# Performance work log

Measured on AMD Instinct MI355X. Metric: run time of the kernel, lower is better.

Reference implementation:

```python
import jax, jax.numpy as jnp
import numpy as np

HIDDEN = 2048
NUM_INPUTS = 4
ACTIVE_IDX = 0
EPS = 1e-6


def rms_norm(x, scale, eps=EPS):
    # Gemma3n RMSNorm: compute in float32, scale by learned per-channel weight.
    x32 = x.astype(jnp.float32)
    inv = jax.lax.rsqrt(jnp.mean(x32 * x32, axis=-1, keepdims=True) + eps)
    return (x32 * inv * scale.astype(jnp.float32)).astype(x.dtype)


def compute_modalities(x, router_norm_scale, router_w):
    # router_norm -> * hidden_size**-1 -> Dense(N) -> tanh (in fp32)
    router_inputs = rms_norm(x, router_norm_scale) * (1.0 / HIDDEN)
    routed = jnp.einsum('bsh,hn->bsn', router_inputs, router_w)
    return jnp.tanh(routed.astype(jnp.float32)).astype(x.dtype)


def setup_inputs() -> dict:
    key = jax.random.key(0)
    k = jax.random.split(key, 7)
    N, B, S, H = NUM_INPUTS, 4, 2048, HIDDEN
    return {
        'hidden_states': jax.random.normal(k[0], (N, B, S, H), dtype=jnp.float32),
        'activated': jax.random.normal(k[1], (B, S, H), dtype=jnp.float32),
        'router_norm_scale': jnp.ones((H,), dtype=jnp.float32) + 0.02 * jax.random.normal(k[2], (H,), dtype=jnp.float32),
        'router_w': 0.02 * jax.random.normal(k[3], (H, N), dtype=jnp.float32),
        'pred_w': 0.02 * jax.random.normal(k[4], (N, N * N), dtype=jnp.float32),
        'corr_w': 0.02 * jax.random.normal(k[5], (N, N), dtype=jnp.float32),
        'correct_output_scale': jax.random.normal(k[6], (H,), dtype=jnp.float32),
    }


def reference(hidden_states, activated, router_norm_scale, router_w, pred_w, corr_w, correct_output_scale):
    N = NUM_INPUTS
    B, S, H = activated.shape

    # ---- predict ----
    mod_p = compute_modalities(hidden_states[ACTIVE_IDX], router_norm_scale, router_w)  # [B,S,N]
    raw = jnp.einsum('bsn,nk->bsk', mod_p, pred_w).reshape(B, S, N, N)  # [B,S,N,N]
    # keras: transpose(raw,(0,1,3,2)) then matmul(hs^(1,2,3,0), .) then transpose back
    # predictions[m,b,s,h] = sum_n hs[n,b,s,h] * raw[b,s,m,n]
    predictions = jnp.einsum('nbsh,bsmn->mbsh', hidden_states, raw) + hidden_states

    # ---- correct ----
    mod_c = compute_modalities(activated, router_norm_scale, router_w)  # [B,S,N]
    innovation = activated - predictions[ACTIVE_IDX]  # [B,S,H]
    coefs = jnp.einsum('bsn,nm->bsm', mod_c, corr_w) + 1.0  # [B,S,N]
    corrected = predictions + innovation[None] * jnp.transpose(coefs, (2, 0, 1))[..., None]

    # ---- scale_corrected_output ----
    return corrected * correct_output_scale
```

## Files before the change

### kernel.cpp

```cpp
#include <hip/hip_runtime.h>

#define HID 2048
#define NTHREADS 256

__global__ __launch_bounds__(NTHREADS) void altup_fused(
    const float* __restrict__ hs,
    const float* __restrict__ act,
    const float* __restrict__ rns,
    const float* __restrict__ rw,
    const float* __restrict__ pw,
    const float* __restrict__ cw,
    const float* __restrict__ cscale,
    float* __restrict__ out,
    int T)
{
    const int t   = blockIdx.x;
    const int tid = threadIdx.x;
    const int h0  = tid * 8;

    __shared__ float s_red[4][10];
    __shared__ float s_raw[16];
    __shared__ float s_coef[4];

    const size_t tok = (size_t)t * HID;
    const size_t strideN = (size_t)T * HID;

    float x0v[8], av[8], nsv[8], wl[32];
    *(float4*)(x0v + 0) = *(const float4*)(hs  + tok + h0 + 0);
    *(float4*)(x0v + 4) = *(const float4*)(hs  + tok + h0 + 4);
    *(float4*)(av  + 0) = *(const float4*)(act + tok + h0 + 0);
    *(float4*)(av  + 4) = *(const float4*)(act + tok + h0 + 4);
    *(float4*)(nsv + 0) = *(const float4*)(rns + h0 + 0);
    *(float4*)(nsv + 4) = *(const float4*)(rns + h0 + 4);
    #pragma unroll
    for (int q = 0; q < 8; ++q)
        *(float4*)(wl + q * 4) = *(const float4*)(rw + (size_t)h0 * 4 + q * 4);

    float r[10];
    #pragma unroll
    for (int k = 0; k < 10; ++k) r[k] = 0.f;
    #pragma unroll
    for (int j = 0; j < 8; ++j) {
        float x0 = x0v[j];
        float a  = av[j];
        float ns = nsv[j];
        r[0] += x0 * x0;
        r[1] += a * a;
        float xs = x0 * ns, as_ = a * ns;
        #pragma unroll
        for (int n = 0; n < 4; ++n) {
            float w = wl[j * 4 + n];
            r[2 + n] += xs  * w;
            r[6 + n] += as_ * w;
        }
    }

    #pragma unroll
    for (int off = 32; off > 0; off >>= 1) {
        #pragma unroll
        for (int k = 0; k < 10; ++k) r[k] += __shfl_down(r[k], off, 64);
    }
    const int wave = tid >> 6, lane = tid & 63;
    if (lane == 0) {
        #pragma unroll
        for (int k = 0; k < 10; ++k) s_red[wave][k] = r[k];
    }
    __syncthreads();

    if (tid == 0) {
        float acc[10];
        #pragma unroll
        for (int k = 0; k < 10; ++k)
            acc[k] = s_red[0][k] + s_red[1][k] + s_red[2][k] + s_red[3][k];
        const float invH = 1.0f / (float)HID;
        float inv_p = rsqrtf(acc[0] * invH + 1e-6f);
        float inv_c = rsqrtf(acc[1] * invH + 1e-6f);
        float mp[4], mc[4];
        #pragma unroll
        for (int n = 0; n < 4; ++n) {
            mp[n] = tanhf(acc[2 + n] * inv_p * invH);
            mc[n] = tanhf(acc[6 + n] * inv_c * invH);
        }
        #pragma unroll
        for (int kk = 0; kk < 16; ++kk) {
            float s = 0.f;
            #pragma unroll
            for (int k = 0; k < 4; ++k) s += mp[k] * pw[k * 16 + kk];
            s_raw[kk] = s;
        }
        #pragma unroll
        for (int m = 0; m < 4; ++m) {
            float s = 1.0f;
            #pragma unroll
            for (int k = 0; k < 4; ++k) s += mc[k] * cw[k * 4 + m];
            s_coef[m] = s;
        }
    }
    __syncthreads();

    float raw[16], coef[4];
    #pragma unroll
    for (int k = 0; k < 16; ++k) raw[k] = s_raw[k];
    #pragma unroll
    for (int m = 0; m < 4; ++m) coef[m] = s_coef[m];

    float x1v[8], x2v[8], x3v[8], csv[8];
    *(float4*)(x1v + 0) = *(const float4*)(hs + 1 * strideN + tok + h0 + 0);
    *(float4*)(x1v + 4) = *(const float4*)(hs + 1 * strideN + tok + h0 + 4);
    *(float4*)(x2v + 0) = *(const float4*)(hs + 2 * strideN + tok + h0 + 0);
    *(float4*)(x2v + 4) = *(const float4*)(hs + 2 * strideN + tok + h0 + 4);
    *(float4*)(x3v + 0) = *(const float4*)(hs + 3 * strideN + tok + h0 + 0);
    *(float4*)(x3v + 4) = *(const float4*)(hs + 3 * strideN + tok + h0 + 4);
    *(float4*)(csv + 0) = *(const float4*)(cscale + h0 + 0);
    *(float4*)(csv + 4) = *(const float4*)(cscale + h0 + 4);

    float o[4][8];
    #pragma unroll
    for (int j = 0; j < 8; ++j) {
        float x[4] = { x0v[j], x1v[j], x2v[j], x3v[j] };
        float a  = av[j];
        float cs = csv[j];
        float pred[4];
        #pragma unroll
        for (int m = 0; m < 4; ++m)
            pred[m] = x[0] * raw[m * 4 + 0] + x[1] * raw[m * 4 + 1]
                    + x[2] * raw[m * 4 + 2] + x[3] * raw[m * 4 + 3] + x[m];
        float innov = a - pred[0];
        #pragma unroll
        for (int m = 0; m < 4; ++m)
            o[m][j] = (pred[m] + innov * coef[m]) * cs;
    }
    #pragma unroll
    for (int m = 0; m < 4; ++m) {
        *(float4*)(out + m * strideN + tok + h0 + 0) = *(const float4*)(o[m] + 0);
        *(float4*)(out + m * strideN + tok + h0 + 4) = *(const float4*)(o[m] + 4);
    }
}

extern "C" void kernel_launch(void* const* d_in, const int* in_sizes, int n_in,
                              void* d_out, int out_size, void* d_ws, size_t ws_size,
                              hipStream_t stream) {
    const float* hs  = (const float*)d_in[0];
    const float* act = (const float*)d_in[1];
    const float* rns = (const float*)d_in[2];
    const float* rw  = (const float*)d_in[3];
    const float* pw  = (const float*)d_in[4];
    const float* cw  = (const float*)d_in[5];
    const float* cs  = (const float*)d_in[6];
    float* out = (float*)d_out;

    const int T = in_sizes[1] / HID;
    altup_fused<<<dim3(T), dim3(NTHREADS), 0, stream>>>(hs, act, rns, rw, pw, cw, cs, out, T);
}
```

Baseline: 565.5 us.

## Coalesce loads, prefetch other streams before reduction, drop serial tid0 stage, nontemporal stores

Each thread now handles two float4 chunks 1024 elements apart instead of eight contiguous floats, so wave accesses are fully coalesced. Loads of the other three hidden-state streams and the output scale are issued before the cross-wave reduction, which lets them overlap the shuffle reduction and barrier. Every thread now computes the tanh and matmul coefficients redundantly, which removes the single-thread stage and the second barrier. Output writes use nontemporal stores to avoid polluting the cache. The cost is higher register pressure and redundant per-thread scalar math.

After: 492.0 us. 1.15x faster.

```diff
diff --git a/kernel.cpp b/kernel.cpp
--- a/kernel.cpp
+++ b/kernel.cpp
@@ -2,6 +2,8 @@
 
 #define HID 2048
 #define NTHREADS 256
+
+typedef float f32x4 __attribute__((ext_vector_type(4)));
 
 __global__ __launch_bounds__(NTHREADS) void altup_fused(
     const float* __restrict__ hs,
@@ -16,125 +18,126 @@
 {
     const int t   = blockIdx.x;
     const int tid = threadIdx.x;
-    const int h0  = tid * 8;
+    const int c0  = tid * 4;
+    const int c1  = c0 + 1024;
 
     __shared__ float s_red[4][10];
-    __shared__ float s_raw[16];
-    __shared__ float s_coef[4];
 
-    const size_t tok = (size_t)t * HID;
+    const size_t tok     = (size_t)t * HID;
     const size_t strideN = (size_t)T * HID;
 
-    float x0v[8], av[8], nsv[8], wl[32];
-    *(float4*)(x0v + 0) = *(const float4*)(hs  + tok + h0 + 0);
-    *(float4*)(x0v + 4) = *(const float4*)(hs  + tok + h0 + 4);
-    *(float4*)(av  + 0) = *(const float4*)(act + tok + h0 + 0);
-    *(float4*)(av  + 4) = *(const float4*)(act + tok + h0 + 4);
-    *(float4*)(nsv + 0) = *(const float4*)(rns + h0 + 0);
-    *(float4*)(nsv + 4) = *(const float4*)(rns + h0 + 4);
+    float x0a[4], x0b[4], aa[4], ab[4], nsa[4], nsb[4], wa[16], wb[16];
+    *(f32x4*)x0a = *(const f32x4*)(hs  + tok + c0);
+    *(f32x4*)x0b = *(const f32x4*)(hs  + tok + c1);
+    *(f32x4*)aa  = *(const f32x4*)(act + tok + c0);
+    *(f32x4*)ab  = *(const f32x4*)(act + tok + c1);
+    *(f32x4*)nsa = *(const f32x4*)(rns + c0);
+    *(f32x4*)nsb = *(const f32x4*)(rns + c1);
     #pragma unroll
-    for (int q = 0; q < 8; ++q)
-        *(float4*)(wl + q * 4) = *(const float4*)(rw + (size_t)h0 * 4 + q * 4);
+    for (int r = 0; r < 4; ++r) {
+        *(f32x4*)(wa + 4 * r) = *(const f32x4*)(rw + (size_t)(c0 + r) * 4);
+        *(f32x4*)(wb + 4 * r) = *(const f32x4*)(rw + (size_t)(c1 + r) * 4);
+    }
 
-    float r[10];
+    float red[10];
     #pragma unroll
-    for (int k = 0; k < 10; ++k) r[k] = 0.f;
+    for (int k = 0; k < 10; ++k) red[k] = 0.f;
     #pragma unroll
-    for (int j = 0; j < 8; ++j) {
-        float x0 = x0v[j];
-        float a  = av[j];
-        float ns = nsv[j];
-        r[0] += x0 * x0;
-        r[1] += a * a;
+    for (int j = 0; j < 4; ++j) {
+        float x0 = x0a[j], a = aa[j], ns = nsa[j];
+        red[0] += x0 * x0;
+        red[1] += a * a;
         float xs = x0 * ns, as_ = a * ns;
         #pragma unroll
         for (int n = 0; n < 4; ++n) {
-            float w = wl[j * 4 + n];
-            r[2 + n] += xs  * w;
-            r[6 + n] += as_ * w;
+            red[2 + n] += xs  * wa[4 * j + n];
+            red[6 + n] += as_ * wa[4 * j + n];
         }
     }
+    #pragma unroll
+    for (int j = 0; j < 4; ++j) {
+        float x0 = x0b[j], a = ab[j], ns = nsb[j];
+        red[0] += x0 * x0;
+        red[1] += a * a;
+        float xs = x0 * ns, as_ = a * ns;
+        #pragma unroll
+        for (int n = 0; n < 4; ++n) {
+            red[2 + n] += xs  * wb[4 * j + n];
+            red[6 + n] += as_ * wb[4 * j + n];
+        }
+    }
+
+    float x1a[4], x1b[4], x2a[4], x2b[4], x3a[4], x3b[4], csa[4], csb[4];
+    *(f32x4*)x1a = *(const f32x4*)(hs + 1 * strideN + tok + c0);
+    *(f32x4*)x1b = *(const f32x4*)(hs + 1 * strideN + tok + c1);
+    *(f32x4*)x2a = *(const f32x4*)(hs + 2 * strideN + tok + c0);
+    *(f32x4*)x2b = *(const f32x4*)(hs + 2 * strideN + tok + c1);
+    *(f32x4*)x3a = *(const f32x4*)(hs + 3 * strideN + tok + c0);
+    *(f32x4*)x3b = *(const f32x4*)(hs + 3 * strideN + tok + c1);
+    *(f32x4*)csa = *(const f32x4*)(cscale + c0);
+    *(f32x4*)csb = *(const f32x4*)(cscale + c1);
 
     #pragma unroll
     for (int off = 32; off > 0; off >>= 1) {
         #pragma unroll
-        for (int k = 0; k < 10; ++k) r[k] += __shfl_down(r[k], off, 64);
+        for (int k = 0; k < 10; ++k) red[k] += __shfl_down(red[k], off, 64);
     }
     const int wave = tid >> 6, lane = tid & 63;
     if (lane == 0) {
         #pragma unroll
-        for (int k = 0; k < 10; ++k) s_red[wave][k] = r[k];
+        for (int k = 0; k < 10; ++k) s_red[wave][k] = red[k];
     }
     __syncthreads();
 
-    if (tid == 0) {
-        float acc[10];
+    float acc[10];
+    #pragma unroll
+    for (int k = 0; k < 10; ++k)
+        acc[k] = s_red[0][k] + s_red[1][k] + s_red[2][k] + s_red[3][k];
+
+    const float invH  = 1.0f / (float)HID;
+    const float inv_p = rsqrtf(acc[0] * invH + 1e-6f) * invH;
+    const float inv_c = rsqrtf(acc[1] * invH + 1e-6f) * invH;
+    float mp[4], mc[4];
+    #pragma unroll
+    for (int n = 0; n < 4; ++n) {
+        mp[n] = tanhf(acc[2 + n] * inv_p);
+        mc[n] = tanhf(acc[6 + n] * inv_c);
+    }
+    float raw[16];
+    #pragma unroll
+    for (int kk = 0; kk < 16; ++kk)
+        raw[kk] = mp[0] * pw[kk]      + mp[1] * pw[16 + kk]
+                + mp[2] * pw[32 + kk] + mp[3] * pw[48 + kk];
+    float coef[4];
+    #pragma unroll
+    for (int m = 0; m < 4; ++m)
+        coef[m] = 1.0f + mc[0] * cw[m]     + mc[1] * cw[4 + m]
+                       + mc[2] * cw[8 + m] + mc[3] * cw[12 + m];
+
+    auto emit = [&](const float* x0, const float* x1, const float* x2,
+                    const float* x3, const float* a, const float* cs,
+                    size_t off) {
+        float o[4][4];
         #pragma unroll
-        for (int k = 0; k < 10; ++k)
-            acc[k] = s_red[0][k] + s_red[1][k] + s_red[2][k] + s_red[3][k];
-        const float invH = 1.0f / (float)HID;
-        float inv_p = rsqrtf(acc[0] * invH + 1e-6f);
-        float inv_c = rsqrtf(acc[1] * invH + 1e-6f);
-        float mp[4], mc[4];
-        #pragma unroll
-        for (int n = 0; n < 4; ++n) {
-            mp[n] = tanhf(acc[2 + n] * inv_p * invH);
-            mc[n] = tanhf(acc[6 + n] * inv_c * invH);
+        for (int j = 0; j < 4; ++j) {
+            float x[4] = { x0[j], x1[j], x2[j], x3[j] };
+            float pred[4];
+            #pragma unroll
+            for (int m = 0; m < 4; ++m)
+                pred[m] = x[0] * raw[4 * m + 0] + x[1] * raw[4 * m + 1]
+                        + x[2] * raw[4 * m + 2] + x[3] * raw[4 * m + 3] + x[m];
+            float innov = a[j] - pred[0];
+            #pragma unroll
+            for (int m = 0; m < 4; ++m)
+                o[m][j] = (pred[m] + innov * coef[m]) * cs[j];
         }
         #pragma unroll
-        for (int kk = 0; kk < 16; ++kk) {
-            float s = 0.f;
-            #pragma unroll
-            for (int k = 0; k < 4; ++k) s += mp[k] * pw[k * 16 + kk];
-            s_raw[kk] = s;
-        }
-        #pragma unroll
-        for (int m = 0; m < 4; ++m) {
-            float s = 1.0f;
-            #pragma unroll
-            for (int k = 0; k < 4; ++k) s += mc[k] * cw[k * 4 + m];
-            s_coef[m] = s;
-        }
-    }
-    __syncthreads();
-
-    float raw[16], coef[4];
-    #pragma unroll
-    for (int k = 0; k < 16; ++k) raw[k] = s_raw[k];
-    #pragma unroll
-    for (int m = 0; m < 4; ++m) coef[m] = s_coef[m];
-
-    float x1v[8], x2v[8], x3v[8], csv[8];
-    *(float4*)(x1v + 0) = *(const float4*)(hs + 1 * strideN + tok + h0 + 0);
-    *(float4*)(x1v + 4) = *(const float4*)(hs + 1 * strideN + tok + h0 + 4);
-    *(float4*)(x2v + 0) = *(const float4*)(hs + 2 * strideN + tok + h0 + 0);
-    *(float4*)(x2v + 4) = *(const float4*)(hs + 2 * strideN + tok + h0 + 4);
-    *(float4*)(x3v + 0) = *(const float4*)(hs + 3 * strideN + tok + h0 + 0);
-    *(float4*)(x3v + 4) = *(const float4*)(hs + 3 * strideN + tok + h0 + 4);
-    *(float4*)(csv + 0) = *(const float4*)(cscale + h0 + 0);
-    *(float4*)(csv + 4) = *(const float4*)(cscale + h0 + 4);
-
-    float o[4][8];
-    #pragma unroll
-    for (int j = 0; j < 8; ++j) {
-        float x[4] = { x0v[j], x1v[j], x2v[j], x3v[j] };
-        float a  = av[j];
-        float cs = csv[j];
-        float pred[4];
-        #pragma unroll
         for (int m = 0; m < 4; ++m)
-            pred[m] = x[0] * raw[m * 4 + 0] + x[1] * raw[m * 4 + 1]
-                    + x[2] * raw[m * 4 + 2] + x[3] * raw[m * 4 + 3] + x[m];
-        float innov = a - pred[0];
-        #pragma unroll
-        for (int m = 0; m < 4; ++m)
-            o[m][j] = (pred[m] + innov * coef[m]) * cs;
-    }
-    #pragma unroll
-    for (int m = 0; m < 4; ++m) {
-        *(float4*)(out + m * strideN + tok + h0 + 0) = *(const float4*)(o[m] + 0);
-        *(float4*)(out + m * strideN + tok + h0 + 4) = *(const float4*)(o[m] + 4);
-    }
+            __builtin_nontemporal_store(*(const f32x4*)o[m],
+                                        (f32x4*)(out + (size_t)m * strideN + off));
+    };
+    emit(x0a, x1a, x2a, x3a, aa, csa, tok + c0);
+    emit(x0b, x1b, x2b, x3b, ab, csb, tok + c1);
 }
 
 extern "C" void kernel_launch(void* const* d_in, const int* in_sizes, int n_in,
```
